# Kernel tuning notes

Measured on AMD Instinct MI355X. Metric: run time of the kernel, lower is better.

The kernel has to match this reference:

```python
import jax, jax.numpy as jnp
import numpy as np

BN_EPS = 1e-5


def setup_inputs() -> dict:
    key = jax.random.key(0)
    ks = jax.random.split(key, 10)
    B, C2, Hh, Ww = 4, 64, 64, 64  # in_channels=128, C/2=64
    C = 2 * C2
    inp = {
        "H": jax.random.normal(ks[0], (B, C2, Hh, Ww), jnp.float32),
        "L": jax.random.normal(ks[1], (B, C2, Hh, Ww), jnp.float32),
        # 1x1 convs stored as [out, in] matrices
        "theta_w": jax.random.normal(ks[2], (C2, C), jnp.float32) * (1.0 / np.sqrt(C)),
        "theta_b": jnp.zeros((C2,), jnp.float32),
        "phi_w": jax.random.normal(ks[3], (C2, C), jnp.float32) * (1.0 / np.sqrt(C)),
        "phi_b": jnp.zeros((C2,), jnp.float32),
        "g_w": jax.random.normal(ks[4], (C2, C2), jnp.float32) * (1.0 / np.sqrt(C2)),
        "g_b": jnp.zeros((C2,), jnp.float32),
        # 3x3 conv of CBR block, OIHW
        "conv_w": jax.random.normal(ks[5], (C2, C2, 3, 3), jnp.float32) * (1.0 / np.sqrt(C2 * 9)),
        "conv_b": jnp.zeros((C2,), jnp.float32),
        # BatchNorm (inference-mode) params
        "bn_gamma": jnp.ones((C2,), jnp.float32),
        "bn_beta": jnp.zeros((C2,), jnp.float32),
        "bn_mean": jnp.zeros((C2,), jnp.float32),
        "bn_var": jnp.ones((C2,), jnp.float32),
    }
    return inp


def reference(H, L, theta_w, theta_b, phi_w, phi_b, g_w, g_b,
              conv_w, conv_b, bn_gamma, bn_beta, bn_mean, bn_var):
    B, C2, h, w = L.shape
    N = h * w
    HL = jnp.concatenate([H, L], axis=1)  # [B, C, h, w]
    # 1x1 conv projections as channel matmuls
    A = jnp.einsum('oc,bchw->bohw', theta_w, HL) + theta_b[:, None, None]  # [B,C2,h,w]
    Bm = jnp.einsum('oc,bchw->bohw', phi_w, HL) + phi_b[:, None, None]
    A = A.reshape(B, C2, N).transpose(0, 2, 1)   # [B, N, C2]
    Bm = Bm.reshape(B, C2, N)                    # [B, C2, N]
    M = jnp.einsum('bnc,bcm->bnm', A, Bm)        # [B, N, N], unscaled
    M = jax.nn.softmax(M, axis=1)                # softmax over FIRST spatial axis (dim=1)
    D = jnp.einsum('oc,bchw->bohw', g_w, L) + g_b[:, None, None]
    D = D.reshape(B, C2, N)                      # [B, C2, N]
    E = jnp.einsum('bcn,bnm->bcm', D, M)         # [B, C2, N]
    E = E.reshape(B, C2, h, w)
    # CBR: conv3x3(pad=1) -> BatchNorm (inference) -> ReLU
    F = jax.lax.conv_general_dilated(
        E, conv_w, window_strides=(1, 1), padding='SAME',
        dimension_numbers=('NCHW', 'OIHW', 'NCHW')) + conv_b[None, :, None, None]
    F = (F - bn_mean[None, :, None, None]) * jax.lax.rsqrt(bn_var + BN_EPS)[None, :, None, None]
    F = F * bn_gamma[None, :, None, None] + bn_beta[None, :, None, None]
    F = jax.nn.relu(F)
    return H + F
```

## Files before the change

kernel.cpp:

```cpp
#include <hip/hip_runtime.h>

typedef __bf16 bf16;
typedef unsigned short u16;
typedef __attribute__((ext_vector_type(8))) __bf16 bf16x8;
typedef __attribute__((ext_vector_type(16))) float f32x16;
typedef __attribute__((ext_vector_type(2))) unsigned int uint2v;
typedef __attribute__((ext_vector_type(4))) unsigned int uint4v;

#define MFMA32(a, b, c) __builtin_amdgcn_mfma_f32_32x32x16_bf16(a, b, c, 0, 0, 0)

__device__ __forceinline__ u16 bbits(float f) {
  bf16 h = (bf16)f;
  return __builtin_bit_cast(u16, h);
}
__device__ __forceinline__ float bf2f(u16 u) {
  return (float)__builtin_bit_cast(bf16, u);
}
__device__ __forceinline__ bf16x8 ldg16(const u16* p) {
  return *reinterpret_cast<const bf16x8*>(p);
}
__device__ __forceinline__ bf16x8 ld_p8(const u16* p) {
  uint2v a = *reinterpret_cast<const uint2v*>(p);
  uint2v b = *reinterpret_cast<const uint2v*>(p + 4);
  uint4v u;
  u.x = a.x; u.y = a.y; u.z = b.x; u.w = b.y;
  return __builtin_bit_cast(bf16x8, u);
}
__device__ __forceinline__ void split8(const float* xv, bf16x8& hi, bf16x8& lo) {
  uint4v hv, lv;
#pragma unroll
  for (int jp = 0; jp < 4; ++jp) {
    float a0 = xv[2 * jp], a1 = xv[2 * jp + 1];
    u16 h0 = bbits(a0), h1 = bbits(a1);
    u16 l0 = bbits(a0 - bf2f(h0)), l1 = bbits(a1 - bf2f(h1));
    unsigned hh = (unsigned)h0 | ((unsigned)h1 << 16);
    unsigned ll = (unsigned)l0 | ((unsigned)l1 << 16);
    if (jp == 0) { hv.x = hh; lv.x = ll; }
    else if (jp == 1) { hv.y = hh; lv.y = ll; }
    else if (jp == 2) { hv.z = hh; lv.z = ll; }
    else { hv.w = hh; lv.w = ll; }
  }
  hi = __builtin_bit_cast(bf16x8, hv);
  lo = __builtin_bit_cast(bf16x8, lv);
}

__global__ __launch_bounds__(256) void pa_prep(
    const float* __restrict__ cw, const float* __restrict__ cbias,
    const float* __restrict__ gamma, const float* __restrict__ beta,
    const float* __restrict__ mean, const float* __restrict__ var,
    const float* __restrict__ tw, const float* __restrict__ pw, const float* __restrict__ gw,
    u16* __restrict__ Wt, float* __restrict__ bnA, float* __restrict__ bnB,
    u16* __restrict__ Wth, u16* __restrict__ Wtl,
    u16* __restrict__ Wph, u16* __restrict__ Wpl,
    u16* __restrict__ Wgh, u16* __restrict__ Wgl) {
  int i = blockIdx.x * 256 + threadIdx.x;
  if (i < 36864) {
    int ci = i & 63, co = (i >> 6) & 63, s = i >> 12;
    Wt[(s * 64 + co) * 64 + ci] = bbits(cw[(co * 64 + ci) * 9 + s]);
  }
  if (i < 8192) {
    float v = tw[i];
    u16 h = bbits(v);
    Wth[i] = h;
    Wtl[i] = bbits(v - bf2f(h));
  } else if (i < 16384) {
    int j = i - 8192;
    float v = pw[j];
    u16 h = bbits(v);
    Wph[j] = h;
    Wpl[j] = bbits(v - bf2f(h));
  } else if (i < 20480) {
    int j = i - 16384;
    float v = gw[j];
    u16 h = bbits(v);
    Wgh[j] = h;
    Wgl[j] = bbits(v - bf2f(h));
  }
  if (i < 64) {
    float rs = rsqrtf(var[i] + 1e-5f);
    float A = gamma[i] * rs;
    bnA[i] = A;
    bnB[i] = (cbias[i] - mean[i]) * A + beta[i];
  }
}

__device__ __forceinline__ void store_qk(const f32x16& a0, const f32x16& a1,
                                         const float* __restrict__ bias,
                                         u16* __restrict__ Hi, u16* __restrict__ Lo,
                                         int p, int q2) {
#pragma unroll
  for (int mt = 0; mt < 2; ++mt) {
    const f32x16& A = mt ? a1 : a0;
#pragma unroll
    for (int rq = 0; rq < 4; ++rq) {
      int chb = mt * 32 + rq * 8 + q2 * 4;
      float4 bb = *reinterpret_cast<const float4*>(bias + chb);
      float v0 = A[rq * 4 + 0] + bb.x;
      float v1 = A[rq * 4 + 1] + bb.y;
      float v2 = A[rq * 4 + 2] + bb.z;
      float v3 = A[rq * 4 + 3] + bb.w;
      u16 h0 = bbits(v0), h1 = bbits(v1), h2 = bbits(v2), h3 = bbits(v3);
      u16 l0 = bbits(v0 - bf2f(h0)), l1 = bbits(v1 - bf2f(h1));
      u16 l2 = bbits(v2 - bf2f(h2)), l3 = bbits(v3 - bf2f(h3));
      uint2v hv, lv;
      hv.x = (unsigned)h0 | ((unsigned)h1 << 16);
      hv.y = (unsigned)h2 | ((unsigned)h3 << 16);
      lv.x = (unsigned)l0 | ((unsigned)l1 << 16);
      lv.y = (unsigned)l2 | ((unsigned)l3 << 16);
      *reinterpret_cast<uint2v*>(Hi + p * 64 + chb) = hv;
      *reinterpret_cast<uint2v*>(Lo + p * 64 + chb) = lv;
    }
  }
}

template <int NS, int STR>
__device__ __forceinline__ void gemm3(const u16* __restrict__ Wh, const u16* __restrict__ Wl,
                                      const bf16x8* Bh, const bf16x8* Bl,
                                      int l31, int q2, f32x16& a0, f32x16& a1) {
#pragma unroll
  for (int s = 0; s < NS; ++s) {
    int ko = s * 16 + q2 * 8;
    bf16x8 w0h = ldg16(Wh + l31 * STR + ko);
    bf16x8 w0l = ldg16(Wl + l31 * STR + ko);
    bf16x8 w1h = ldg16(Wh + (32 + l31) * STR + ko);
    bf16x8 w1l = ldg16(Wl + (32 + l31) * STR + ko);
    a0 = MFMA32(w0h, Bh[s], a0);
    a0 = MFMA32(w0h, Bl[s], a0);
    a0 = MFMA32(w0l, Bh[s], a0);
    a1 = MFMA32(w1h, Bh[s], a1);
    a1 = MFMA32(w1h, Bl[s], a1);
    a1 = MFMA32(w1l, Bh[s], a1);
  }
}

__global__ __launch_bounds__(384, 2) void pa_proj(
    const float* __restrict__ H, const float* __restrict__ L,
    const float* __restrict__ tb, const float* __restrict__ pb, const float* __restrict__ gb,
    const u16* __restrict__ Wth, const u16* __restrict__ Wtl,
    const u16* __restrict__ Wph, const u16* __restrict__ Wpl,
    const u16* __restrict__ Wgh, const u16* __restrict__ Wgl,
    u16* __restrict__ Qh, u16* __restrict__ Ql,
    u16* __restrict__ Kh, u16* __restrict__ Kl, u16* __restrict__ V) {
  int b = blockIdx.x >> 6;
  int tile = blockIdx.x & 63;
  int w = threadIdx.x >> 6;
  int lane = threadIdx.x & 63;
  int l31 = lane & 31, q2 = lane >> 5;
  int half = w & 1, role = w >> 1;
  int n0 = tile * 64 + half * 32;
  int n = n0 + l31;
  int p0 = b * 4096 + n0;

  if (role < 2) {
    bf16x8 Bh[8], Bl[8];
#pragma unroll
    for (int s = 0; s < 8; ++s) {
      const float* src = (s < 4) ? (H + (b * 64 + s * 16) * 4096)
                                 : (L + (b * 64 + (s - 4) * 16) * 4096);
      const float* pp = src + (q2 * 8) * 4096 + n;
      float xv[8];
#pragma unroll
      for (int j = 0; j < 8; ++j) xv[j] = pp[j * 4096];
      split8(xv, Bh[s], Bl[s]);
    }
    const u16* Wh = role ? Wph : Wth;
    const u16* Wl = role ? Wpl : Wtl;
    const float* bias = role ? pb : tb;
    u16* Oh = role ? Qh : Kh;
    u16* Ol = role ? Ql : Kl;
    f32x16 a0 = {}, a1 = {};
    gemm3<8, 128>(Wh, Wl, Bh, Bl, l31, q2, a0, a1);
    store_qk(a0, a1, bias, Oh, Ol, p0 + l31, q2);
  } else {
    bf16x8 Bh[4], Bl[4];
#pragma unroll
    for (int s = 0; s < 4; ++s) {
      const float* pp = L + (b * 64 + s * 16 + q2 * 8) * 4096 + n;
      float xv[8];
#pragma unroll
      for (int j = 0; j < 8; ++j) xv[j] = pp[j * 4096];
      split8(xv, Bh[s], Bl[s]);
    }
    f32x16 a0 = {}, a1 = {};
    gemm3<4, 64>(Wgh, Wgl, Bh, Bl, l31, q2, a0, a1);
#pragma unroll
    for (int mt = 0; mt < 2; ++mt) {
      const f32x16& A = mt ? a1 : a0;
#pragma unroll
      for (int rq = 0; rq < 4; ++rq) {
        int chb = mt * 32 + rq * 8 + q2 * 4;
        float4 bb = *reinterpret_cast<const float4*>(gb + chb);
        V[(b * 64 + chb + 0) * 4096 + n] = bbits(A[rq * 4 + 0] + bb.x);
        V[(b * 64 + chb + 1) * 4096 + n] = bbits(A[rq * 4 + 1] + bb.y);
        V[(b * 64 + chb + 2) * 4096 + n] = bbits(A[rq * 4 + 2] + bb.z);
        V[(b * 64 + chb + 3) * 4096 + n] = bbits(A[rq * 4 + 3] + bb.w);
      }
    }
  }
}

__global__ __launch_bounds__(512, 2) void pa_flash(
    const u16* __restrict__ Qh, const u16* __restrict__ Ql,
    const u16* __restrict__ Kh, const u16* __restrict__ Kl,
    const u16* __restrict__ V, u16* __restrict__ E) {
  __shared__ __align__(16) char smem[54272];
  u16* Pb = (u16*)smem;
  u16* Qld = (u16*)(smem + 36864);
  float* Obuf = (float*)smem;
  float* MLm = (float*)(smem + 17152);
  float* MLl = (float*)(smem + 19200);
  float* Lst = (float*)(smem + 21248);

  int tid = threadIdx.x;
  int w = tid >> 6, lane = tid & 63;
  int l31 = lane & 31, q2 = lane >> 5;
  int b = blockIdx.x >> 6, y = blockIdx.x & 63;
  int m0 = y * 64;
  int bq = b * 4096;

  {
    int m = tid >> 3, c0 = (tid & 7) * 8;
    int gidx = (bq + m0 + m) * 64 + c0;
    bf16x8 vh = ldg16(Qh + gidx);
    bf16x8 vl = ldg16(Ql + gidx);
    uint4v uh = __builtin_bit_cast(uint4v, vh);
    uint4v ul = __builtin_bit_cast(uint4v, vl);
    u16* dh = Qld + m * 68 + c0;
    uint2v t0; t0.x = uh.x; t0.y = uh.y;
    uint2v t1; t1.x = uh.z; t1.y = uh.w;
    *reinterpret_cast<uint2v*>(dh) = t0;
    *reinterpret_cast<uint2v*>(dh + 4) = t1;
    u16* dl = Qld + 4352 + m * 68 + c0;
    uint2v t2; t2.x = ul.x; t2.y = ul.y;
    uint2v t3; t3.x = ul.z; t3.y = ul.w;
    *reinterpret_cast<uint2v*>(dl) = t2;
    *reinterpret_cast<uint2v*>(dl + 4) = t3;
  }
  __syncthreads();

  f32x16 accO[2][2] = {};
  float Mm[2] = {0.f, 0.f};
  float Ll[2] = {0.f, 0.f};
  u16* mypb = Pb + w * (64 * 36);

  bf16x8 khb[2][4], klb[2][4];
#pragma unroll
  for (int kc = 0; kc < 4; ++kc) {
    int idx = (bq + w * 32 + l31) * 64 + kc * 16 + q2 * 8;
    khb[0][kc] = ldg16(Kh + idx);
    klb[0][kc] = ldg16(Kl + idx);
  }

#pragma unroll 2
  for (int it = 0; it < 16; ++it) {
    int cur = it & 1, nxt = cur ^ 1;
    int n0 = it * 256 + w * 32;
    int n0n = ((it < 15) ? (it + 1) : it) * 256 + w * 32;

#pragma unroll
    for (int kc = 0; kc < 4; ++kc) {
      int idx = (bq + n0n + l31) * 64 + kc * 16 + q2 * 8;
      khb[nxt][kc] = ldg16(Kh + idx);
      klb[nxt][kc] = ldg16(Kl + idx);
    }
    bf16x8 vf[2][2];
#pragma unroll
    for (int cbi = 0; cbi < 2; ++cbi)
#pragma unroll
      for (int kch = 0; kch < 2; ++kch)
        vf[cbi][kch] = ldg16(V + (b * 64 + cbi * 32 + l31) * 4096 + n0 + kch * 16 + q2 * 8);

#pragma unroll
    for (int mb = 0; mb < 2; ++mb) {
      f32x16 a = {}, b2 = {};
#pragma unroll
      for (int kc = 0; kc < 2; ++kc) {
        const u16* qrow = Qld + (mb * 32 + l31) * 68 + kc * 16 + q2 * 8;
        bf16x8 qh8 = ld_p8(qrow);
        bf16x8 ql8 = ld_p8(qrow + 4352);
        a = MFMA32(khb[cur][kc], qh8, a);
        a = MFMA32(khb[cur][kc], ql8, a);
        a = MFMA32(klb[cur][kc], qh8, a);
      }
#pragma unroll
      for (int kc = 2; kc < 4; ++kc) {
        const u16* qrow = Qld + (mb * 32 + l31) * 68 + kc * 16 + q2 * 8;
        bf16x8 qh8 = ld_p8(qrow);
        bf16x8 ql8 = ld_p8(qrow + 4352);
        b2 = MFMA32(khb[cur][kc], qh8, b2);
        b2 = MFMA32(khb[cur][kc], ql8, b2);
        b2 = MFMA32(klb[cur][kc], qh8, b2);
      }
      float sv[16];
#pragma unroll
      for (int r = 0; r < 16; ++r) sv[r] = a[r] + b2[r];
      if (it == 0) {
        float tmax = sv[0];
#pragma unroll
        for (int r = 1; r < 16; ++r) tmax = fmaxf(tmax, sv[r]);
        tmax = fmaxf(tmax, __shfl_xor(tmax, 32, 64));
        Mm[mb] = tmax;
      }
      float pv[16];
      float psum = 0.f;
#pragma unroll
      for (int r = 0; r < 16; ++r) {
        pv[r] = __expf(sv[r] - Mm[mb]);
        psum += pv[r];
      }
      psum += __shfl_xor(psum, 32, 64);
      Ll[mb] += psum;
      u16* prow = mypb + (mb * 32 + l31) * 36;
#pragma unroll
      for (int rq = 0; rq < 4; ++rq) {
        unsigned lo = (unsigned)bbits(pv[rq * 4 + 0]) | ((unsigned)bbits(pv[rq * 4 + 1]) << 16);
        unsigned hi = (unsigned)bbits(pv[rq * 4 + 2]) | ((unsigned)bbits(pv[rq * 4 + 3]) << 16);
        uint2v uu;
        uu.x = lo;
        uu.y = hi;
        *reinterpret_cast<uint2v*>(prow + rq * 8 + q2 * 4) = uu;
      }
      bf16x8 p0 = ld_p8(prow + q2 * 8);
      bf16x8 p1 = ld_p8(prow + 16 + q2 * 8);
      accO[0][mb] = MFMA32(vf[0][0], p0, accO[0][mb]);
      accO[0][mb] = MFMA32(vf[0][1], p1, accO[0][mb]);
      accO[1][mb] = MFMA32(vf[1][0], p0, accO[1][mb]);
      accO[1][mb] = MFMA32(vf[1][1], p1, accO[1][mb]);
    }
  }

  __syncthreads();
  if (q2 == 0) {
#pragma unroll
    for (int mb = 0; mb < 2; ++mb) {
      MLm[(w * 2 + mb) * 32 + l31] = Mm[mb];
      MLl[(w * 2 + mb) * 32 + l31] = Ll[mb];
    }
  }
  __syncthreads();
  float mysc[2];
#pragma unroll
  for (int mb = 0; mb < 2; ++mb) {
    float M = MLm[(0 * 2 + mb) * 32 + l31];
    for (int ww = 1; ww < 8; ++ww) M = fmaxf(M, MLm[(ww * 2 + mb) * 32 + l31]);
    float ls = 0.f;
    for (int ww = 0; ww < 8; ++ww)
      ls += MLl[(ww * 2 + mb) * 32 + l31] * __expf(MLm[(ww * 2 + mb) * 32 + l31] - M);
    mysc[mb] = __expf(Mm[mb] - M);
    if (w == 0 && q2 == 0) Lst[mb * 32 + l31] = ls;
  }
  for (int ww = 0; ww < 8; ++ww) {
    if (w == ww) {
#pragma unroll
      for (int cbi = 0; cbi < 2; ++cbi)
#pragma unroll
        for (int mb = 0; mb < 2; ++mb) {
          float sc = mysc[mb];
#pragma unroll
          for (int r = 0; r < 16; ++r) {
            int c = cbi * 32 + (r & 3) + 8 * (r >> 2) + 4 * q2;
            int m = mb * 32 + l31;
            float* dst = &Obuf[c * 67 + m];
            float v = accO[cbi][mb][r] * sc;
            if (ww == 0)
              *dst = v;
            else
              *dst += v;
          }
        }
    }
    __syncthreads();
  }
  int em = tid >> 3, ec0 = (tid & 7) * 8;
  float invl = 1.0f / Lst[em];
  float vals[8];
#pragma unroll
  for (int j = 0; j < 8; ++j) vals[j] = Obuf[(ec0 + j) * 67 + em] * invl;
  uint4v u0;
  u0.x = (unsigned)bbits(vals[0]) | ((unsigned)bbits(vals[1]) << 16);
  u0.y = (unsigned)bbits(vals[2]) | ((unsigned)bbits(vals[3]) << 16);
  u0.z = (unsigned)bbits(vals[4]) | ((unsigned)bbits(vals[5]) << 16);
  u0.w = (unsigned)bbits(vals[6]) | ((unsigned)bbits(vals[7]) << 16);
  u16* ep = E + (bq + m0 + em) * 64 + ec0;
  *reinterpret_cast<uint4v*>(ep) = u0;
}

__global__ __launch_bounds__(256) void pa_conv(
    const u16* __restrict__ E, const u16* __restrict__ Wt,
    const float* __restrict__ bnA, const float* __restrict__ bnB,
    const float* __restrict__ H, float* __restrict__ out) {
  __shared__ u16 Er[3][66 * 68];
  int tid = threadIdx.x;
  int blk = blockIdx.x;
  int b = blk >> 6, y = blk & 63;
  int lane = tid & 63;
  int l31 = lane & 31, q2 = lane >> 5;
  int wv = tid >> 6;
  int cbi = wv >> 1, mb = wv & 1;
  int s0 = (y == 0) ? 1 : 0;
  int s1 = (y == 63) ? 1 : 2;

  for (int s = s0; s <= s1; ++s) {
    int yy = y + s - 1;
#pragma unroll
    for (int rep = 0; rep < 2; ++rep) {
      int id = rep * 256 + tid;
      int x = id >> 3, co = (id & 7) * 8;
      const uint2v* src = reinterpret_cast<const uint2v*>(E + ((b * 4096 + yy * 64 + x) * 64 + co));
      uint2v a = src[0], b4 = src[1];
      u16* d = &Er[s][(x + 1) * 68 + co];
      *reinterpret_cast<uint2v*>(d) = a;
      *reinterpret_cast<uint2v*>(d + 4) = b4;
    }
  }
  if (tid < 96) {
    int s = tid >> 5, side = (tid >> 4) & 1, co = (tid & 15) * 4;
    uint2v z;
    z.x = 0;
    z.y = 0;
    *reinterpret_cast<uint2v*>(&Er[s][(side ? 65 : 0) * 68 + co]) = z;
  }
  __syncthreads();

  f32x16 acc = {};
  for (int s = s0; s <= s1; ++s) {
#pragma unroll
    for (int dx = 0; dx < 3; ++dx)
#pragma unroll
      for (int kc = 0; kc < 4; ++kc) {
        bf16x8 a = ldg16(Wt + ((s * 3 + dx) * 64 + cbi * 32 + l31) * 64 + kc * 16 + q2 * 8);
        const u16* pbr = &Er[s][(mb * 32 + l31 + dx) * 68 + kc * 16 + q2 * 8];
        bf16x8 bb = ld_p8(pbr);
        acc = MFMA32(a, bb, acc);
      }
  }
#pragma unroll
  for (int r = 0; r < 16; ++r) {
    int c = cbi * 32 + (r & 3) + 8 * (r >> 2) + 4 * q2;
    int x = mb * 32 + l31;
    float v = acc[r] * bnA[c] + bnB[c];
    v = fmaxf(v, 0.f);
    int idx = ((b * 64 + c) * 64 + y) * 64 + x;
    out[idx] = H[idx] + v;
  }
}

extern "C" void kernel_launch(void* const* d_in, const int* in_sizes, int n_in,
                              void* d_out, int out_size, void* d_ws, size_t ws_size,
                              hipStream_t stream) {
  (void)in_sizes; (void)n_in; (void)out_size; (void)ws_size;
  const float* H = (const float*)d_in[0];
  const float* L = (const float*)d_in[1];
  const float* tw = (const float*)d_in[2];
  const float* tb = (const float*)d_in[3];
  const float* pw = (const float*)d_in[4];
  const float* pb = (const float*)d_in[5];
  const float* gw = (const float*)d_in[6];
  const float* gb = (const float*)d_in[7];
  const float* cw = (const float*)d_in[8];
  const float* cb = (const float*)d_in[9];
  const float* gamma = (const float*)d_in[10];
  const float* beta = (const float*)d_in[11];
  const float* mean = (const float*)d_in[12];
  const float* var = (const float*)d_in[13];

  const int NC = 16384 * 64;
  u16* Qh = (u16*)d_ws;
  u16* Ql = Qh + NC;
  u16* Kh = Ql + NC;
  u16* Kl = Kh + NC;
  u16* Vv = Kl + NC;
  u16* Eb = Vv + NC;
  u16* Wt = Eb + NC;
  float* bnA = (float*)(Wt + 36864);
  float* bnB = bnA + 64;
  u16* Wth = (u16*)(bnB + 64);
  u16* Wtl = Wth + 8192;
  u16* Wph = Wtl + 8192;
  u16* Wpl = Wph + 8192;
  u16* Wgh = Wpl + 8192;
  u16* Wgl = Wgh + 4096;

  pa_prep<<<144, 256, 0, stream>>>(cw, cb, gamma, beta, mean, var, tw, pw, gw,
                                   Wt, bnA, bnB, Wth, Wtl, Wph, Wpl, Wgh, Wgl);
  pa_proj<<<256, 384, 0, stream>>>(H, L, tb, pb, gb, Wth, Wtl, Wph, Wpl, Wgh, Wgl,
                                   Qh, Ql, Kh, Kl, Vv);
  pa_flash<<<256, 512, 0, stream>>>(Qh, Ql, Kh, Kl, Vv, Eb);
  pa_conv<<<256, 256, 0, stream>>>(Eb, Wt, bnA, bnB, H, (float*)d_out);
}
```

Before: 158.0 us.

## Pre-swizzle Q/K/V into MFMA fragment layout and shrink flash tiles

Projection outputs Q, K, V and the projection weights are written in a fragment-swizzled layout, so each lane loads its MFMA operand with one contiguous 16-byte load. The Q smem staging and K double buffering are removed. The flash kernel now uses 32-row query tiles over 512 blocks with smaller shared memory and higher occupancy. K's low-precision half is dropped, cutting the QK^T product from three to two MFMA passes per chunk. This trades some score precision for fewer MFMAs and less memory traffic, and it loses the explicit K prefetch.

```diff
diff --git a/kernel.cpp b/kernel.cpp
--- a/kernel.cpp
+++ b/kernel.cpp
@@ -43,6 +43,7 @@
   hi = __builtin_bit_cast(bf16x8, hv);
   lo = __builtin_bit_cast(bf16x8, lv);
 }
+
 
 __global__ __launch_bounds__(256) void pa_prep(
     const float* __restrict__ cw, const float* __restrict__ cbias,
@@ -58,23 +59,26 @@
     int ci = i & 63, co = (i >> 6) & 63, s = i >> 12;
     Wt[(s * 64 + co) * 64 + ci] = bbits(cw[(co * 64 + ci) * 9 + s]);
   }
-  if (i < 8192) {
-    float v = tw[i];
+  if (i < 16384) {
+    int ii = i & 8191;
+    int j = ii & 7, l = (ii >> 3) & 63, f = ii >> 9;
+    int out = (f & 1) * 32 + (l & 31);
+    int in = (f >> 1) * 16 + (l >> 5) * 8 + j;
+    const float* W = (i < 8192) ? tw : pw;
+    float v = W[out * 128 + in];
     u16 h = bbits(v);
-    Wth[i] = h;
-    Wtl[i] = bbits(v - bf2f(h));
-  } else if (i < 16384) {
-    int j = i - 8192;
-    float v = pw[j];
+    u16 lo = bbits(v - bf2f(h));
+    if (i < 8192) { Wth[ii] = h; Wtl[ii] = lo; }
+    else { Wph[ii] = h; Wpl[ii] = lo; }
+  } else if (i < 20480) {
+    int ii = i - 16384;
+    int j = ii & 7, l = (ii >> 3) & 63, f = ii >> 9;
+    int out = (f & 1) * 32 + (l & 31);
+    int in = (f >> 1) * 16 + (l >> 5) * 8 + j;
+    float v = gw[out * 64 + in];
     u16 h = bbits(v);
-    Wph[j] = h;
-    Wpl[j] = bbits(v - bf2f(h));
-  } else if (i < 20480) {
-    int j = i - 16384;
-    float v = gw[j];
-    u16 h = bbits(v);
-    Wgh[j] = h;
-    Wgl[j] = bbits(v - bf2f(h));
+    Wgh[ii] = h;
+    Wgl[ii] = bbits(v - bf2f(h));
   }
   if (i < 64) {
     float rs = rsqrtf(var[i] + 1e-5f);
@@ -84,46 +88,50 @@
   }
 }
 
-__device__ __forceinline__ void store_qk(const f32x16& a0, const f32x16& a1,
-                                         const float* __restrict__ bias,
-                                         u16* __restrict__ Hi, u16* __restrict__ Lo,
-                                         int p, int q2) {
+template <bool LO>
+__device__ __forceinline__ void store_qk_swz(const f32x16& a0, const f32x16& a1,
+                                             const float* __restrict__ bias,
+                                             u16* __restrict__ Hi, u16* __restrict__ Lo,
+                                             int base, int l31, int q2) {
 #pragma unroll
   for (int mt = 0; mt < 2; ++mt) {
     const f32x16& A = mt ? a1 : a0;
 #pragma unroll
     for (int rq = 0; rq < 4; ++rq) {
-      int chb = mt * 32 + rq * 8 + q2 * 4;
-      float4 bb = *reinterpret_cast<const float4*>(bias + chb);
+      int ch = mt * 32 + rq * 8 + q2 * 4;
+      float4 bb = *reinterpret_cast<const float4*>(bias + ch);
       float v0 = A[rq * 4 + 0] + bb.x;
       float v1 = A[rq * 4 + 1] + bb.y;
       float v2 = A[rq * 4 + 2] + bb.z;
       float v3 = A[rq * 4 + 3] + bb.w;
+      int off = base + ((mt * 2 + (rq >> 1)) * 64 + l31 + 32 * (rq & 1)) * 8 + q2 * 4;
       u16 h0 = bbits(v0), h1 = bbits(v1), h2 = bbits(v2), h3 = bbits(v3);
-      u16 l0 = bbits(v0 - bf2f(h0)), l1 = bbits(v1 - bf2f(h1));
-      u16 l2 = bbits(v2 - bf2f(h2)), l3 = bbits(v3 - bf2f(h3));
-      uint2v hv, lv;
+      uint2v hv;
       hv.x = (unsigned)h0 | ((unsigned)h1 << 16);
       hv.y = (unsigned)h2 | ((unsigned)h3 << 16);
-      lv.x = (unsigned)l0 | ((unsigned)l1 << 16);
-      lv.y = (unsigned)l2 | ((unsigned)l3 << 16);
-      *reinterpret_cast<uint2v*>(Hi + p * 64 + chb) = hv;
-      *reinterpret_cast<uint2v*>(Lo + p * 64 + chb) = lv;
-    }
-  }
-}
-
-template <int NS, int STR>
+      *reinterpret_cast<uint2v*>(Hi + off) = hv;
+      if (LO) {
+        u16 l0 = bbits(v0 - bf2f(h0)), l1 = bbits(v1 - bf2f(h1));
+        u16 l2 = bbits(v2 - bf2f(h2)), l3 = bbits(v3 - bf2f(h3));
+        uint2v lv;
+        lv.x = (unsigned)l0 | ((unsigned)l1 << 16);
+        lv.y = (unsigned)l2 | ((unsigned)l3 << 16);
+        *reinterpret_cast<uint2v*>(Lo + off) = lv;
+      }
+    }
+  }
+}
+
+template <int NS>
 __device__ __forceinline__ void gemm3(const u16* __restrict__ Wh, const u16* __restrict__ Wl,
                                       const bf16x8* Bh, const bf16x8* Bl,
-                                      int l31, int q2, f32x16& a0, f32x16& a1) {
+                                      int lane, f32x16& a0, f32x16& a1) {
 #pragma unroll
   for (int s = 0; s < NS; ++s) {
-    int ko = s * 16 + q2 * 8;
-    bf16x8 w0h = ldg16(Wh + l31 * STR + ko);
-    bf16x8 w0l = ldg16(Wl + l31 * STR + ko);
-    bf16x8 w1h = ldg16(Wh + (32 + l31) * STR + ko);
-    bf16x8 w1l = ldg16(Wl + (32 + l31) * STR + ko);
+    bf16x8 w0h = ldg16(Wh + ((s * 2 + 0) * 64 + lane) * 8);
+    bf16x8 w0l = ldg16(Wl + ((s * 2 + 0) * 64 + lane) * 8);
+    bf16x8 w1h = ldg16(Wh + ((s * 2 + 1) * 64 + lane) * 8);
+    bf16x8 w1l = ldg16(Wl + ((s * 2 + 1) * 64 + lane) * 8);
     a0 = MFMA32(w0h, Bh[s], a0);
     a0 = MFMA32(w0h, Bl[s], a0);
     a0 = MFMA32(w0l, Bh[s], a0);
@@ -140,16 +148,16 @@
     const u16* __restrict__ Wph, const u16* __restrict__ Wpl,
     const u16* __restrict__ Wgh, const u16* __restrict__ Wgl,
     u16* __restrict__ Qh, u16* __restrict__ Ql,
-    u16* __restrict__ Kh, u16* __restrict__ Kl, u16* __restrict__ V) {
+    u16* __restrict__ Kh, u16* __restrict__ V) {
   int b = blockIdx.x >> 6;
-  int tile = blockIdx.x & 63;
+  int tile64 = blockIdx.x & 63;
   int w = threadIdx.x >> 6;
   int lane = threadIdx.x & 63;
   int l31 = lane & 31, q2 = lane >> 5;
   int half = w & 1, role = w >> 1;
-  int n0 = tile * 64 + half * 32;
-  int n = n0 + l31;
-  int p0 = b * 4096 + n0;
+  int tile32 = tile64 * 2 + half;
+  int n = tile32 * 32 + l31;
+  int base = tile32 * 2048;
 
   if (role < 2) {
     bf16x8 Bh[8], Bl[8];
@@ -163,14 +171,14 @@
       for (int j = 0; j < 8; ++j) xv[j] = pp[j * 4096];
       split8(xv, Bh[s], Bl[s]);
     }
-    const u16* Wh = role ? Wph : Wth;
-    const u16* Wl = role ? Wpl : Wtl;
-    const float* bias = role ? pb : tb;
-    u16* Oh = role ? Qh : Kh;
-    u16* Ol = role ? Ql : Kl;
     f32x16 a0 = {}, a1 = {};
-    gemm3<8, 128>(Wh, Wl, Bh, Bl, l31, q2, a0, a1);
-    store_qk(a0, a1, bias, Oh, Ol, p0 + l31, q2);
+    if (role == 0) {
+      gemm3<8>(Wth, Wtl, Bh, Bl, lane, a0, a1);
+      store_qk_swz<false>(a0, a1, tb, Kh + b * 262144, (u16*)nullptr, base, l31, q2);
+    } else {
+      gemm3<8>(Wph, Wpl, Bh, Bl, lane, a0, a1);
+      store_qk_swz<true>(a0, a1, pb, Qh + b * 262144, Ql + b * 262144, base, l31, q2);
+    }
   } else {
     bf16x8 Bh[4], Bl[4];
 #pragma unroll
@@ -182,207 +190,154 @@
       split8(xv, Bh[s], Bl[s]);
     }
     f32x16 a0 = {}, a1 = {};
-    gemm3<4, 64>(Wgh, Wgl, Bh, Bl, l31, q2, a0, a1);
+    gemm3<4>(Wgh, Wgl, Bh, Bl, lane, a0, a1);
+    u16* Vb = V + b * 262144;
+    int kch = (l31 >> 4) & 1, q2v = (l31 >> 3) & 1, jn = l31 & 7;
 #pragma unroll
     for (int mt = 0; mt < 2; ++mt) {
       const f32x16& A = mt ? a1 : a0;
 #pragma unroll
       for (int rq = 0; rq < 4; ++rq) {
-        int chb = mt * 32 + rq * 8 + q2 * 4;
-        float4 bb = *reinterpret_cast<const float4*>(gb + chb);
-        V[(b * 64 + chb + 0) * 4096 + n] = bbits(A[rq * 4 + 0] + bb.x);
-        V[(b * 64 + chb + 1) * 4096 + n] = bbits(A[rq * 4 + 1] + bb.y);
-        V[(b * 64 + chb + 2) * 4096 + n] = bbits(A[rq * 4 + 2] + bb.z);
-        V[(b * 64 + chb + 3) * 4096 + n] = bbits(A[rq * 4 + 3] + bb.w);
+        int ch = mt * 32 + rq * 8 + q2 * 4;
+        float4 bb = *reinterpret_cast<const float4*>(gb + ch);
+        float vv[4] = {A[rq * 4 + 0] + bb.x, A[rq * 4 + 1] + bb.y,
+                       A[rq * 4 + 2] + bb.z, A[rq * 4 + 3] + bb.w};
+#pragma unroll
+        for (int i2 = 0; i2 < 4; ++i2) {
+          int c31 = rq * 8 + q2 * 4 + i2;
+          int lane_v = c31 + 32 * q2v;
+          Vb[(((tile32 * 2 + kch) * 2 + mt) * 64 + lane_v) * 8 + jn] = bbits(vv[i2]);
+        }
       }
     }
   }
 }
 
-__global__ __launch_bounds__(512, 2) void pa_flash(
-    const u16* __restrict__ Qh, const u16* __restrict__ Ql,
-    const u16* __restrict__ Kh, const u16* __restrict__ Kl,
-    const u16* __restrict__ V, u16* __restrict__ E) {
-  __shared__ __align__(16) char smem[54272];
+__global__ __launch_bounds__(512, 4) void pa_flash(
+    const u16* __restrict__ Qhg, const u16* __restrict__ Qlg,
+    const u16* __restrict__ Khg, const u16* __restrict__ Vg, u16* __restrict__ E) {
+  __shared__ __align__(16) char smem[18432];
   u16* Pb = (u16*)smem;
-  u16* Qld = (u16*)(smem + 36864);
   float* Obuf = (float*)smem;
-  float* MLm = (float*)(smem + 17152);
-  float* MLl = (float*)(smem + 19200);
-  float* Lst = (float*)(smem + 21248);
+  float* MLm = (float*)(smem + 8448);
+  float* MLl = (float*)(smem + 9472);
+  float* Lst = (float*)(smem + 10496);
 
   int tid = threadIdx.x;
   int w = tid >> 6, lane = tid & 63;
   int l31 = lane & 31, q2 = lane >> 5;
-  int b = blockIdx.x >> 6, y = blockIdx.x & 63;
-  int m0 = y * 64;
+  int b = blockIdx.x >> 7, mt = blockIdx.x & 127;
+  int m0 = mt * 32;
   int bq = b * 4096;
-
-  {
-    int m = tid >> 3, c0 = (tid & 7) * 8;
-    int gidx = (bq + m0 + m) * 64 + c0;
-    bf16x8 vh = ldg16(Qh + gidx);
-    bf16x8 vl = ldg16(Ql + gidx);
-    uint4v uh = __builtin_bit_cast(uint4v, vh);
-    uint4v ul = __builtin_bit_cast(uint4v, vl);
-    u16* dh = Qld + m * 68 + c0;
-    uint2v t0; t0.x = uh.x; t0.y = uh.y;
-    uint2v t1; t1.x = uh.z; t1.y = uh.w;
-    *reinterpret_cast<uint2v*>(dh) = t0;
-    *reinterpret_cast<uint2v*>(dh + 4) = t1;
-    u16* dl = Qld + 4352 + m * 68 + c0;
-    uint2v t2; t2.x = ul.x; t2.y = ul.y;
-    uint2v t3; t3.x = ul.z; t3.y = ul.w;
-    *reinterpret_cast<uint2v*>(dl) = t2;
-    *reinterpret_cast<uint2v*>(dl + 4) = t3;
-  }
-  __syncthreads();
-
-  f32x16 accO[2][2] = {};
-  float Mm[2] = {0.f, 0.f};
-  float Ll[2] = {0.f, 0.f};
-  u16* mypb = Pb + w * (64 * 36);
-
-  bf16x8 khb[2][4], klb[2][4];
+  const u16* Qb = Qhg + b * 262144;
+  const u16* Qlb = Qlg + b * 262144;
+  const u16* Kb = Khg + b * 262144;
+  const u16* Vb = Vg + b * 262144;
+
+  bf16x8 qh[4], ql[4];
 #pragma unroll
   for (int kc = 0; kc < 4; ++kc) {
-    int idx = (bq + w * 32 + l31) * 64 + kc * 16 + q2 * 8;
-    khb[0][kc] = ldg16(Kh + idx);
-    klb[0][kc] = ldg16(Kl + idx);
-  }
-
-#pragma unroll 2
+    qh[kc] = ldg16(Qb + ((mt * 4 + kc) * 64 + lane) * 8);
+    ql[kc] = ldg16(Qlb + ((mt * 4 + kc) * 64 + lane) * 8);
+  }
+
+  f32x16 accO[2] = {};
+  float Mm = 0.f, Ll = 0.f;
+  u16* mypb = Pb + w * (32 * 36);
+  u16* prow = mypb + l31 * 36;
+
+#pragma unroll 1
   for (int it = 0; it < 16; ++it) {
-    int cur = it & 1, nxt = cur ^ 1;
-    int n0 = it * 256 + w * 32;
-    int n0n = ((it < 15) ? (it + 1) : it) * 256 + w * 32;
-
+    int tile = it * 8 + w;
+
+    bf16x8 kh[4];
+#pragma unroll
+    for (int kc = 0; kc < 4; ++kc) kh[kc] = ldg16(Kb + ((tile * 4 + kc) * 64 + lane) * 8);
+    bf16x8 vf[2][2];
+#pragma unroll
+    for (int kch = 0; kch < 2; ++kch)
+#pragma unroll
+      for (int cbi = 0; cbi < 2; ++cbi)
+        vf[cbi][kch] = ldg16(Vb + (((tile * 2 + kch) * 2 + cbi) * 64 + lane) * 8);
+
+    f32x16 a = {};
 #pragma unroll
     for (int kc = 0; kc < 4; ++kc) {
-      int idx = (bq + n0n + l31) * 64 + kc * 16 + q2 * 8;
-      khb[nxt][kc] = ldg16(Kh + idx);
-      klb[nxt][kc] = ldg16(Kl + idx);
-    }
-    bf16x8 vf[2][2];
-#pragma unroll
-    for (int cbi = 0; cbi < 2; ++cbi)
-#pragma unroll
-      for (int kch = 0; kch < 2; ++kch)
-        vf[cbi][kch] = ldg16(V + (b * 64 + cbi * 32 + l31) * 4096 + n0 + kch * 16 + q2 * 8);
-
-#pragma unroll
-    for (int mb = 0; mb < 2; ++mb) {
-      f32x16 a = {}, b2 = {};
-#pragma unroll
-      for (int kc = 0; kc < 2; ++kc) {
-        const u16* qrow = Qld + (mb * 32 + l31) * 68 + kc * 16 + q2 * 8;
-        bf16x8 qh8 = ld_p8(qrow);
-        bf16x8 ql8 = ld_p8(qrow + 4352);
-        a = MFMA32(khb[cur][kc], qh8, a);
-        a = MFMA32(khb[cur][kc], ql8, a);
-        a = MFMA32(klb[cur][kc], qh8, a);
-      }
-#pragma unroll
-      for (int kc = 2; kc < 4; ++kc) {
-        const u16* qrow = Qld + (mb * 32 + l31) * 68 + kc * 16 + q2 * 8;
-        bf16x8 qh8 = ld_p8(qrow);
-        bf16x8 ql8 = ld_p8(qrow + 4352);
-        b2 = MFMA32(khb[cur][kc], qh8, b2);
-        b2 = MFMA32(khb[cur][kc], ql8, b2);
-        b2 = MFMA32(klb[cur][kc], qh8, b2);
-      }
-      float sv[16];
-#pragma unroll
-      for (int r = 0; r < 16; ++r) sv[r] = a[r] + b2[r];
-      if (it == 0) {
-        float tmax = sv[0];
-#pragma unroll
-        for (int r = 1; r < 16; ++r) tmax = fmaxf(tmax, sv[r]);
-        tmax = fmaxf(tmax, __shfl_xor(tmax, 32, 64));
-        Mm[mb] = tmax;
-      }
-      float pv[16];
-      float psum = 0.f;
-#pragma unroll
-      for (int r = 0; r < 16; ++r) {
-        pv[r] = __expf(sv[r] - Mm[mb]);
-        psum += pv[r];
-      }
-      psum += __shfl_xor(psum, 32, 64);
-      Ll[mb] += psum;
-      u16* prow = mypb + (mb * 32 + l31) * 36;
-#pragma unroll
-      for (int rq = 0; rq < 4; ++rq) {
-        unsigned lo = (unsigned)bbits(pv[rq * 4 + 0]) | ((unsigned)bbits(pv[rq * 4 + 1]) << 16);
-        unsigned hi = (unsigned)bbits(pv[rq * 4 + 2]) | ((unsigned)bbits(pv[rq * 4 + 3]) << 16);
-        uint2v uu;
-        uu.x = lo;
-        uu.y = hi;
-        *reinterpret_cast<uint2v*>(prow + rq * 8 + q2 * 4) = uu;
-      }
-      bf16x8 p0 = ld_p8(prow + q2 * 8);
-      bf16x8 p1 = ld_p8(prow + 16 + q2 * 8);
-      accO[0][mb] = MFMA32(vf[0][0], p0, accO[0][mb]);
-      accO[0][mb] = MFMA32(vf[0][1], p1, accO[0][mb]);
-      accO[1][mb] = MFMA32(vf[1][0], p0, accO[1][mb]);
-      accO[1][mb] = MFMA32(vf[1][1], p1, accO[1][mb]);
-    }
+      a = MFMA32(kh[kc], qh[kc], a);
+      a = MFMA32(kh[kc], ql[kc], a);
+    }
+    if (it == 0) {
+      float tmax = a[0];
+#pragma unroll
+      for (int r = 1; r < 16; ++r) tmax = fmaxf(tmax, a[r]);
+      tmax = fmaxf(tmax, __shfl_xor(tmax, 32, 64));
+      Mm = tmax;
+    }
+    float pv[16];
+    float psum = 0.f;
+#pragma unroll
+    for (int r = 0; r < 16; ++r) {
+      pv[r] = __expf(a[r] - Mm);
+      psum += pv[r];
+    }
+    psum += __shfl_xor(psum, 32, 64);
+    Ll += psum;
+#pragma unroll
+    for (int rq = 0; rq < 4; ++rq) {
+      unsigned lo = (unsigned)bbits(pv[rq * 4 + 0]) | ((unsigned)bbits(pv[rq * 4 + 1]) << 16);
+      unsigned hi = (unsigned)bbits(pv[rq * 4 + 2]) | ((unsigned)bbits(pv[rq * 4 + 3]) << 16);
+      uint2v uu;
+      uu.x = lo;
+      uu.y = hi;
+      *reinterpret_cast<uint2v*>(prow + rq * 8 + q2 * 4) = uu;
+    }
+    bf16x8 p0 = ld_p8(prow + q2 * 8);
+    bf16x8 p1 = ld_p8(prow + 16 + q2 * 8);
+    accO[0] = MFMA32(vf[0][0], p0, accO[0]);
+    accO[0] = MFMA32(vf[0][1], p1, accO[0]);
+    accO[1] = MFMA32(vf[1][0], p0, accO[1]);
+    accO[1] = MFMA32(vf[1][1], p1, accO[1]);
   }
 
   __syncthreads();
   if (q2 == 0) {
-#pragma unroll
-    for (int mb = 0; mb < 2; ++mb) {
-      MLm[(w * 2 + mb) * 32 + l31] = Mm[mb];
-      MLl[(w * 2 + mb) * 32 + l31] = Ll[mb];
-    }
+    MLm[w * 32 + l31] = Mm;
+    MLl[w * 32 + l31] = Ll;
   }
   __syncthreads();
-  float mysc[2];
-#pragma unroll
-  for (int mb = 0; mb < 2; ++mb) {
-    float M = MLm[(0 * 2 + mb) * 32 + l31];
-    for (int ww = 1; ww < 8; ++ww) M = fmaxf(M, MLm[(ww * 2 + mb) * 32 + l31]);
-    float ls = 0.f;
-    for (int ww = 0; ww < 8; ++ww)
-      ls += MLl[(ww * 2 + mb) * 32 + l31] * __expf(MLm[(ww * 2 + mb) * 32 + l31] - M);
-    mysc[mb] = __expf(Mm[mb] - M);
-    if (w == 0 && q2 == 0) Lst[mb * 32 + l31] = ls;
-  }
+  float M = MLm[l31];
+  for (int ww = 1; ww < 8; ++ww) M = fmaxf(M, MLm[ww * 32 + l31]);
+  float ls = 0.f;
+  for (int ww = 0; ww < 8; ++ww) ls += MLl[ww * 32 + l31] * __expf(MLm[ww * 32 + l31] - M);
+  float mysc = __expf(Mm - M);
+  if (w == 0 && q2 == 0) Lst[l31] = ls;
   for (int ww = 0; ww < 8; ++ww) {
     if (w == ww) {
 #pragma unroll
       for (int cbi = 0; cbi < 2; ++cbi)
 #pragma unroll
-        for (int mb = 0; mb < 2; ++mb) {
-          float sc = mysc[mb];
-#pragma unroll
-          for (int r = 0; r < 16; ++r) {
-            int c = cbi * 32 + (r & 3) + 8 * (r >> 2) + 4 * q2;
-            int m = mb * 32 + l31;
-            float* dst = &Obuf[c * 67 + m];
-            float v = accO[cbi][mb][r] * sc;
-            if (ww == 0)
-              *dst = v;
-            else
-              *dst += v;
-          }
+        for (int r = 0; r < 16; ++r) {
+          int c = cbi * 32 + (r & 3) + 8 * (r >> 2) + 4 * q2;
+          float* dst = &Obuf[c * 33 + l31];
+          float v = accO[cbi][r] * mysc;
+          if (ww == 0)
+            *dst = v;
+          else
+            *dst += v;
         }
     }
     __syncthreads();
   }
-  int em = tid >> 3, ec0 = (tid & 7) * 8;
+  int em = tid >> 4, ec0 = (tid & 15) * 4;
   float invl = 1.0f / Lst[em];
-  float vals[8];
-#pragma unroll
-  for (int j = 0; j < 8; ++j) vals[j] = Obuf[(ec0 + j) * 67 + em] * invl;
-  uint4v u0;
-  u0.x = (unsigned)bbits(vals[0]) | ((unsigned)bbits(vals[1]) << 16);
-  u0.y = (unsigned)bbits(vals[2]) | ((unsigned)bbits(vals[3]) << 16);
-  u0.z = (unsigned)bbits(vals[4]) | ((unsigned)bbits(vals[5]) << 16);
-  u0.w = (unsigned)bbits(vals[6]) | ((unsigned)bbits(vals[7]) << 16);
-  u16* ep = E + (bq + m0 + em) * 64 + ec0;
-  *reinterpret_cast<uint4v*>(ep) = u0;
+  float v0 = Obuf[(ec0 + 0) * 33 + em] * invl;
+  float v1 = Obuf[(ec0 + 1) * 33 + em] * invl;
+  float v2 = Obuf[(ec0 + 2) * 33 + em] * invl;
+  float v3 = Obuf[(ec0 + 3) * 33 + em] * invl;
+  uint2v u0;
+  u0.x = (unsigned)bbits(v0) | ((unsigned)bbits(v1) << 16);
+  u0.y = (unsigned)bbits(v2) | ((unsigned)bbits(v3) << 16);
+  *reinterpret_cast<uint2v*>(E + (bq + m0 + em) * 64 + ec0) = u0;
 }
 
 __global__ __launch_bounds__(256) void pa_conv(
@@ -468,8 +423,7 @@
   u16* Qh = (u16*)d_ws;
   u16* Ql = Qh + NC;
   u16* Kh = Ql + NC;
-  u16* Kl = Kh + NC;
-  u16* Vv = Kl + NC;
+  u16* Vv = Kh + NC;
   u16* Eb = Vv + NC;
   u16* Wt = Eb + NC;
   float* bnA = (float*)(Wt + 36864);
@@ -484,7 +438,7 @@
   pa_prep<<<144, 256, 0, stream>>>(cw, cb, gamma, beta, mean, var, tw, pw, gw,
                                    Wt, bnA, bnB, Wth, Wtl, Wph, Wpl, Wgh, Wgl);
   pa_proj<<<256, 384, 0, stream>>>(H, L, tb, pb, gb, Wth, Wtl, Wph, Wpl, Wgh, Wgl,
-                                   Qh, Ql, Kh, Kl, Vv);
-  pa_flash<<<256, 512, 0, stream>>>(Qh, Ql, Kh, Kl, Vv, Eb);
+                                   Qh, Ql, Kh, Vv);
+  pa_flash<<<512, 512, 0, stream>>>(Qh, Ql, Kh, Vv, Eb);
   pa_conv<<<256, 256, 0, stream>>>(Eb, Wt, bnA, bnB, H, (float*)d_out);
 }
```

Measured after the change: 133.4 us. 1.18x faster.
